# Optimization experiments

Measured on AMD Instinct MI355X. Metric: run time of the kernel, lower is better.

The kernel has to match this reference:

```python
import jax, jax.numpy as jnp
import numpy as np

B, N, C = 8, 4096, 256
HID = 256          # HGNN conv hidden width
MLP_HID = 64       # final_mlp_hidden_width


def setup_inputs() -> dict:
    key = jax.random.key(0)
    ks = jax.random.split(key, 10)
    s = lambda fan_in: 1.0 / np.sqrt(fan_in)
    states = jax.random.normal(ks[0], (B, N, C), dtype=jnp.float32)
    # symmetric-normalized hypergraph Laplacian-like propagation matrix [N, N]
    A = jax.random.uniform(ks[1], (N, N), dtype=jnp.float32)
    A = 0.5 * (A + A.T)
    d = jnp.sum(A, axis=1)
    G = A / jnp.sqrt(d[:, None] * d[None, :])
    W1 = jax.random.uniform(ks[2], (C, HID), jnp.float32, -s(C), s(C))
    b1 = jnp.zeros((HID,), jnp.float32)
    W2 = jax.random.uniform(ks[3], (HID, HID), jnp.float32, -s(HID), s(HID))
    b2 = jnp.zeros((HID,), jnp.float32)
    Wm1 = jax.random.uniform(ks[4], (HID, MLP_HID), jnp.float32, -s(HID), s(HID))
    bm1 = jnp.zeros((MLP_HID,), jnp.float32)
    Wm2 = jax.random.uniform(ks[5], (MLP_HID, 1), jnp.float32, -s(MLP_HID), s(MLP_HID))
    bm2 = jnp.zeros((1,), jnp.float32)
    return {"states": states, "G": G, "W1": W1, "b1": b1, "W2": W2,
            "b2": b2, "Wm1": Wm1, "bm1": bm1, "Wm2": Wm2, "bm2": bm2}


def reference(states, G, W1, b1, W2, b2, Wm1, bm1, Wm2, bm2):
    # HGNN conv 1: G @ (X W1 + b1), ReLU.  states: [B,N,C]
    h = jnp.einsum('nm,bmh->bnh', G, states @ W1 + b1)
    h = jax.nn.relu(h)
    # HGNN conv 2
    h = jnp.einsum('nm,bmh->bnh', G, h @ W2 + b2)
    h = jax.nn.relu(h)
    # final MLP: hidden -> 64 -> 1 (per-node scalar state value)
    h = jax.nn.relu(h @ Wm1 + bm1)
    return h @ Wm2 + bm2  # [B, N, 1]
```

## Files before the change

kernel.cpp:

```cpp
#include <hip/hip_runtime.h>

#define N_NODES 4096
#define C_IN    256
#define HID     256
#define BATCH   8
#define R_TOT   32768

typedef unsigned short u16;
typedef short s8v  __attribute__((ext_vector_type(8)));
typedef float f4v  __attribute__((ext_vector_type(4)));
typedef u16   u16x4 __attribute__((ext_vector_type(4)));

#define MFMA(a,b,c) __builtin_amdgcn_mfma_f32_16x16x32_bf16((a),(b),(c),0,0,0)

__device__ __forceinline__ u16 bf_rne(float x) {
    unsigned u = __float_as_uint(x);
    u += 0x7fffu + ((u >> 16) & 1u);
    return (u16)(u >> 16);
}
__device__ __forceinline__ float bf_f(u16 h) {
    return __uint_as_float(((unsigned)h) << 16);
}
__device__ __forceinline__ void split2f(float x, u16& h, u16& l) {
    h = bf_rne(x);
    l = bf_rne(x - bf_f(h));
}

__device__ __forceinline__ void glds16(const void* g, void* l) {
    __builtin_amdgcn_global_load_lds(
        (const __attribute__((address_space(1))) void*)g,
        (__attribute__((address_space(3))) void*)l, 16, 0, 0);
}


__global__ void splitGX_k(const float* __restrict__ G, u16* __restrict__ Gh,
                          const float* __restrict__ X, u16* __restrict__ Xh) {
    const int nG = 4194304;
    const int nTot = nG + 2097152;
    int i = blockIdx.x * blockDim.x + threadIdx.x;
    const int stride = gridDim.x * blockDim.x;
    for (; i < nTot; i += stride) {
        const float4* src; u16x4* dst; int j;
        if (i < nG) { src = (const float4*)G; dst = (u16x4*)Gh; j = i; }
        else        { src = (const float4*)X; dst = (u16x4*)Xh; j = i - nG; }
        float4 x = src[j];
        u16x4 hh;
        hh[0] = bf_rne(x.x); hh[1] = bf_rne(x.y);
        hh[2] = bf_rne(x.z); hh[3] = bf_rne(x.w);
        dst[j] = hh;
    }
}

__global__ void splitT2_k(const float* __restrict__ W1, u16* __restrict__ W1th,
                          u16* __restrict__ W1tl, const float* __restrict__ W2,
                          u16* __restrict__ W2th, u16* __restrict__ W2tl) {
    const float* in = blockIdx.y ? W2 : W1;
    u16* oh = blockIdx.y ? W2th : W1th;
    u16* ol = blockIdx.y ? W2tl : W1tl;
    const int c = blockIdx.x;
    const int h = threadIdx.x;
    float v = in[c * 256 + h];
    u16 hi, lo; split2f(v, hi, lo);
    oh[h * 256 + c] = hi;
    ol[h * 256 + c] = lo;
}

__global__ __launch_bounds__(256, 2) void gemm_small_k(
    const u16* __restrict__ Ah, const u16* __restrict__ Al,
    const u16* __restrict__ Bh,
    const float* __restrict__ bias, u16* __restrict__ Oh)
{
    __shared__ u16 sAh[4096], sAl[4096], sBh[4096];
    const int tid = threadIdx.x;
    const int w = tid >> 6, lane = tid & 63;
    const int i0 = blockIdx.x * 128;
    const int r0 = blockIdx.y * 128;
    const int lr = lane & 15, lk = lane >> 4;
    const int wr = (w >> 1) * 64, wc = (w & 1) * 64;
    const int kslot = (lk ^ ((lr >> 1) & 3)) * 8;
    const int cb = ((lane & 3) ^ ((lane >> 3) & 3)) * 8;

    const u16 *pAh[2], *pAl[2], *pBh[2];
#pragma unroll
    for (int j = 0; j < 2; ++j) {
        const int ra = i0 + (w * 2 + j) * 16 + (lane >> 2);
        pAh[j] = Ah + (size_t)ra * 256 + cb;
        pAl[j] = Al + (size_t)ra * 256 + cb;
        const int rb = r0 + (w * 2 + j) * 16 + (lane >> 2);
        pBh[j] = Bh + (size_t)rb * 256 + cb;
    }

    f4v acc[4][4] = {};

    for (int kt = 0; kt < 8; ++kt) {
#pragma unroll
        for (int j = 0; j < 2; ++j) {
            glds16(pAh[j] + kt * 32, sAh + (w * 2 + j) * 512);
            glds16(pAl[j] + kt * 32, sAl + (w * 2 + j) * 512);
            glds16(pBh[j] + kt * 32, sBh + (w * 2 + j) * 512);
        }
        __syncthreads();

        s8v fah[4], fal[4], fbh[4];
#pragma unroll
        for (int m = 0; m < 4; ++m) {
            fah[m] = *(const s8v*)(sAh + (wr + m * 16 + lr) * 32 + kslot);
            fal[m] = *(const s8v*)(sAl + (wr + m * 16 + lr) * 32 + kslot);
            fbh[m] = *(const s8v*)(sBh + (wc + m * 16 + lr) * 32 + kslot);
        }
#pragma unroll
        for (int m = 0; m < 4; ++m)
#pragma unroll
            for (int n = 0; n < 4; ++n)
                acc[m][n] = MFMA(fah[m], fbh[n], acc[m][n]);
#pragma unroll
        for (int m = 0; m < 4; ++m)
#pragma unroll
            for (int n = 0; n < 4; ++n)
                acc[m][n] = MFMA(fal[m], fbh[n], acc[m][n]);
        __syncthreads();
    }

#pragma unroll
    for (int m = 0; m < 4; ++m) {
#pragma unroll
        for (int q = 0; q < 4; ++q) {
            const int rowg = i0 + wr + m * 16 + lk * 4 + q;
            const float bv = bias[rowg];
#pragma unroll
            for (int n = 0; n < 4; ++n) {
                const int colg = r0 + wc + n * 16 + lr;
                float v = acc[m][n][q] + bv;
                Oh[(size_t)rowg * R_TOT + colg] = bf_rne(v);
            }
        }
    }
}

__global__ __launch_bounds__(512, 2) void gemm_big_k(
    const u16* __restrict__ Gh, const u16* __restrict__ Th,
    u16* __restrict__ Hh)
{
    extern __shared__ u16 lds[];
    const int tid = threadIdx.x;
    const int w = tid >> 6, l = tid & 63;
    const int n0 = blockIdx.x * 256;
    const int h0 = blockIdx.y * 128;
    const int b  = blockIdx.z;
    const int lr = l & 15, lk = l >> 4;
    const int wm = w >> 1, wn = w & 1;
    const int sl0 = ((lk)     ^ (lr & 7)) * 8;
    const int sl1 = ((4 + lk) ^ (lr & 7)) * 8;

    const int srow  = l >> 3;
    const int sslot = ((l & 7) ^ srow) * 8;

    const u16* pA0 = Gh + (size_t)(n0 + 8 * w        + srow) * 4096 + sslot;
    const u16* pA1 = Gh + (size_t)(n0 + 8 * (w + 8)  + srow) * 4096 + sslot;
    const u16* pA2 = Gh + (size_t)(n0 + 8 * (w + 16) + srow) * 4096 + sslot;
    const u16* pA3 = Gh + (size_t)(n0 + 8 * (w + 24) + srow) * 4096 + sslot;
    const u16* pB0 = Th + (size_t)(h0 + 8 * w       + srow) * R_TOT + (size_t)b * 4096 + sslot;
    const u16* pB1 = Th + (size_t)(h0 + 8 * (w + 8) + srow) * R_TOT + (size_t)b * 4096 + sslot;

    const int dA0 = w * 512, dA1 = (w + 8) * 512, dA2 = (w + 16) * 512, dA3 = (w + 24) * 512;
    const int dB0 = 16384 + w * 512, dB1 = 16384 + (w + 8) * 512;

    f4v acc[4][4] = {};

#define STAGE6(STG) do {                                                       \
    u16* Ls = lds + (STG) * 24576;                                             \
    glds16(pA0, Ls + dA0); glds16(pA1, Ls + dA1);                              \
    glds16(pA2, Ls + dA2); glds16(pA3, Ls + dA3);                              \
    glds16(pB0, Ls + dB0); glds16(pB1, Ls + dB1);                              \
    pA0 += 64; pA1 += 64; pA2 += 64; pA3 += 64; pB0 += 64; pB1 += 64;          \
} while (0)

#define KTILE(CUR, STG, DO_STAGE, VMODE) do {                                  \
    const u16* Lc = lds + (CUR) * 24576;                                       \
    u16* Ls = lds + (STG) * 24576;                                             \
                                  \
    { s8v fa[4], fb[4];                                                        \
      _Pragma("unroll") for (int m = 0; m < 4; ++m)                            \
          fa[m] = *(const s8v*)(Lc + (wm * 64 + m * 16 + lr) * 64 + sl0);      \
      _Pragma("unroll") for (int n = 0; n < 4; ++n)                            \
          fb[n] = *(const s8v*)(Lc + 16384 + (wn * 64 + n * 16 + lr) * 64 + sl0); \
      if (DO_STAGE) { glds16(pA0, Ls + dA0); glds16(pA1, Ls + dA1);            \
                      glds16(pB0, Ls + dB0); }                                 \
      __builtin_amdgcn_s_barrier();                                            \
      __builtin_amdgcn_s_setprio(1);                                           \
      _Pragma("unroll") for (int m = 0; m < 4; ++m)                            \
          _Pragma("unroll") for (int n = 0; n < 4; ++n)                        \
              acc[m][n] = MFMA(fa[m], fb[n], acc[m][n]);                       \
      __builtin_amdgcn_s_setprio(0);                                           \
      __builtin_amdgcn_s_barrier(); }                                          \
                     \
    { s8v fa[4], fb[4];                                                        \
      _Pragma("unroll") for (int m = 0; m < 4; ++m)                            \
          fa[m] = *(const s8v*)(Lc + (wm * 64 + m * 16 + lr) * 64 + sl1);      \
      _Pragma("unroll") for (int n = 0; n < 4; ++n)                            \
          fb[n] = *(const s8v*)(Lc + 16384 + (wn * 64 + n * 16 + lr) * 64 + sl1); \
      if (DO_STAGE) { glds16(pA2, Ls + dA2); glds16(pA3, Ls + dA3);            \
                      glds16(pB1, Ls + dB1);                                   \
                      pA0 += 64; pA1 += 64; pA2 += 64; pA3 += 64;              \
                      pB0 += 64; pB1 += 64; }                                  \
      __builtin_amdgcn_s_barrier();                                            \
      __builtin_amdgcn_s_setprio(1);                                           \
      _Pragma("unroll") for (int m = 0; m < 4; ++m)                            \
          _Pragma("unroll") for (int n = 0; n < 4; ++n)                        \
              acc[m][n] = MFMA(fa[m], fb[n], acc[m][n]);                       \
      __builtin_amdgcn_s_setprio(0); }                                         \
    if (VMODE == 0)      asm volatile("s_waitcnt vmcnt(6)" ::: "memory");      \
    else if (VMODE == 1) asm volatile("s_waitcnt vmcnt(0)" ::: "memory");      \
    if (VMODE != 2) __builtin_amdgcn_s_barrier();                              \
    __builtin_amdgcn_sched_barrier(0);                                         \
} while (0)

    STAGE6(0);
    STAGE6(1);
    asm volatile("s_waitcnt vmcnt(6)" ::: "memory");
    __builtin_amdgcn_s_barrier();
    __builtin_amdgcn_sched_barrier(0);

    for (int it = 0; it < 20; ++it) {
        KTILE(0, 2, 1, 0);
        KTILE(1, 0, 1, 0);
        KTILE(2, 1, 1, 0);
    }
    KTILE(0, 2, 1, 0);
    KTILE(1, 0, 1, 0);
    KTILE(2, 1, 0, 1);
    KTILE(0, 2, 0, 2);

#undef STAGE6
#undef KTILE

    const size_t obase = ((size_t)b * 4096 + n0 + wm * 64 + lk * 4) * 256
                       + h0 + wn * 64 + lr;
#pragma unroll
    for (int m = 0; m < 4; ++m)
#pragma unroll
        for (int n = 0; n < 4; ++n)
#pragma unroll
            for (int q = 0; q < 4; ++q) {
                float v = acc[m][n][q];
                v = v > 0.f ? v : 0.f;
                Hh[obase + (size_t)(m * 16 + q) * 256 + n * 16] = bf_rne(v);
            }
}

__global__ __launch_bounds__(256) void mlp_k(
    const u16* __restrict__ Hh, const float* __restrict__ Wm1,
    const float* __restrict__ bm1, const float* __restrict__ Wm2,
    const float* __restrict__ bm2, float* __restrict__ out)
{
    __shared__ u16 sB[16384];
    const int tid = threadIdx.x;
    const int w = tid >> 6, l = tid & 63;
    const int lr = l & 15, lk = l >> 4;

    for (int idx = tid; idx < 16384; idx += 256) {
        const int col = idx & 63, k = idx >> 6;
        const int slot = (k >> 3) ^ (col & 7);
        sB[col * 256 + slot * 8 + (k & 7)] = bf_rne(Wm1[k * 64 + col]);
    }
    __syncthreads();

    float bm1v[4], w2v[4];
#pragma unroll
    for (int n = 0; n < 4; ++n) {
        bm1v[n] = bm1[n * 16 + lr];
        w2v[n]  = Wm2[n * 16 + lr];
    }
    const float b2v = bm2[0];

    const int rowbase = blockIdx.x * 128 + w * 32;
    f4v acc[2][4] = {};
#pragma unroll
    for (int ks = 0; ks < 8; ++ks) {
        s8v fa[2], fb[4];
#pragma unroll
        for (int m = 0; m < 2; ++m)
            fa[m] = *(const s8v*)(Hh + (size_t)(rowbase + m * 16 + lr) * 256 + ks * 32 + lk * 8);
        const int slot = ((ks * 4 + lk) ^ (lr & 7)) * 8;
#pragma unroll
        for (int n = 0; n < 4; ++n)
            fb[n] = *(const s8v*)(sB + (n * 16 + lr) * 256 + slot);
#pragma unroll
        for (int m = 0; m < 2; ++m)
#pragma unroll
            for (int n = 0; n < 4; ++n)
                acc[m][n] = MFMA(fa[m], fb[n], acc[m][n]);
    }

#pragma unroll
    for (int m = 0; m < 2; ++m)
#pragma unroll
        for (int q = 0; q < 4; ++q) {
            float p = 0.f;
#pragma unroll
            for (int n = 0; n < 4; ++n) {
                float v = acc[m][n][q] + bm1v[n];
                v = v > 0.f ? v : 0.f;
                p += v * w2v[n];
            }
#pragma unroll
            for (int mask = 1; mask < 16; mask <<= 1)
                p += __shfl_xor(p, mask);
            if (lr == 0)
                out[rowbase + m * 16 + lk * 4 + q] = p + b2v;
        }
}

extern "C" void kernel_launch(void* const* d_in, const int* in_sizes, int n_in,
                              void* d_out, int out_size, void* d_ws, size_t ws_size,
                              hipStream_t stream) {
    (void)in_sizes; (void)n_in; (void)out_size; (void)ws_size;
    const float* X   = (const float*)d_in[0];
    const float* G   = (const float*)d_in[1];
    const float* W1  = (const float*)d_in[2];
    const float* b1  = (const float*)d_in[3];
    const float* W2  = (const float*)d_in[4];
    const float* b2  = (const float*)d_in[5];
    const float* Wm1 = (const float*)d_in[6];
    const float* bm1 = (const float*)d_in[7];
    const float* Wm2 = (const float*)d_in[8];
    const float* bm2 = (const float*)d_in[9];
    float* out = (float*)d_out;

    char* ws = (char*)d_ws;
    u16* Gh   = (u16*)(ws);
    u16* W1th = (u16*)(ws + 67108864u);
    u16* W1tl = (u16*)(ws + 67239936u);
    u16* W2th = (u16*)(ws + 67371008u);
    u16* W2tl = (u16*)(ws + 67502080u);
    u16* Tth  = (u16*)(ws + 67633152u);
    u16* XHh  = (u16*)(ws + 101187584u);

    splitGX_k<<<3072, 256, 0, stream>>>(G, Gh, X, XHh);
    splitT2_k<<<dim3(256, 2), 256, 0, stream>>>(W1, W1th, W1tl, W2, W2th, W2tl);

    gemm_small_k<<<dim3(2, 256), 256, 0, stream>>>(W1th, W1tl, XHh, b1, Tth);
    gemm_big_k<<<dim3(16, 2, 8), 512, 147456, stream>>>(Gh, Tth, XHh);
    gemm_small_k<<<dim3(2, 256), 256, 0, stream>>>(W2th, W2tl, XHh, b2, Tth);
    gemm_big_k<<<dim3(16, 2, 8), 512, 147456, stream>>>(Gh, Tth, XHh);
    mlp_k<<<256, 256, 0, stream>>>(XHh, Wm1, bm1, Wm2, bm2, out);
}
```

Before: 191.1 us.

## Load B operand directly from global into registers, keep only A in LDS

New measurement: 367.4 us. +92.2%, slower.

```diff
diff --git a/kernel.cpp b/kernel.cpp
--- a/kernel.cpp
+++ b/kernel.cpp
@@ -155,83 +155,92 @@
     const int srow  = l >> 3;
     const int sslot = ((l & 7) ^ srow) * 8;
 
-    const u16* pA0 = Gh + (size_t)(n0 + 8 * w        + srow) * 4096 + sslot;
-    const u16* pA1 = Gh + (size_t)(n0 + 8 * (w + 8)  + srow) * 4096 + sslot;
-    const u16* pA2 = Gh + (size_t)(n0 + 8 * (w + 16) + srow) * 4096 + sslot;
-    const u16* pA3 = Gh + (size_t)(n0 + 8 * (w + 24) + srow) * 4096 + sslot;
-    const u16* pB0 = Th + (size_t)(h0 + 8 * w       + srow) * R_TOT + (size_t)b * 4096 + sslot;
-    const u16* pB1 = Th + (size_t)(h0 + 8 * (w + 8) + srow) * R_TOT + (size_t)b * 4096 + sslot;
-
+    const u16* pA0 = Gh + (size_t)(n0 + 8 * w + srow) * 4096 + sslot;
+    const u16* pA1 = pA0 + (size_t)64  * 4096;
+    const u16* pA2 = pA0 + (size_t)128 * 4096;
+    const u16* pA3 = pA0 + (size_t)192 * 4096;
     const int dA0 = w * 512, dA1 = (w + 8) * 512, dA2 = (w + 16) * 512, dA3 = (w + 24) * 512;
-    const int dB0 = 16384 + w * 512, dB1 = 16384 + (w + 8) * 512;
+
+    const u16* pB[4];
+#pragma unroll
+    for (int n = 0; n < 4; ++n)
+        pB[n] = Th + (size_t)(h0 + wn * 64 + n * 16 + lr) * R_TOT
+                   + (size_t)b * 4096 + lk * 8;
 
     f4v acc[4][4] = {};
-
-#define STAGE6(STG) do {                                                       \
-    u16* Ls = lds + (STG) * 24576;                                             \
+    s8v bbA[8], bbB[8];
+
+#define STAGEA(STG) do {                                                       \
+    u16* Ls = lds + (STG) * 16384;                                             \
     glds16(pA0, Ls + dA0); glds16(pA1, Ls + dA1);                              \
     glds16(pA2, Ls + dA2); glds16(pA3, Ls + dA3);                              \
-    glds16(pB0, Ls + dB0); glds16(pB1, Ls + dB1);                              \
-    pA0 += 64; pA1 += 64; pA2 += 64; pA3 += 64; pB0 += 64; pB1 += 64;          \
+    pA0 += 64; pA1 += 64; pA2 += 64; pA3 += 64;                                \
 } while (0)
 
-#define KTILE(CUR, STG, DO_STAGE, VMODE) do {                                  \
-    const u16* Lc = lds + (CUR) * 24576;                                       \
-    u16* Ls = lds + (STG) * 24576;                                             \
-                                  \
-    { s8v fa[4], fb[4];                                                        \
+#define KTILE(CUR, STG, BBC, BBN, DO_STAGE, DO_B, VMODE) do {                  \
+    const u16* Lc = lds + (CUR) * 16384;                                       \
+                           \
+    { s8v fa[4];                                                               \
       _Pragma("unroll") for (int m = 0; m < 4; ++m)                            \
           fa[m] = *(const s8v*)(Lc + (wm * 64 + m * 16 + lr) * 64 + sl0);      \
-      _Pragma("unroll") for (int n = 0; n < 4; ++n)                            \
-          fb[n] = *(const s8v*)(Lc + 16384 + (wn * 64 + n * 16 + lr) * 64 + sl0); \
-      if (DO_STAGE) { glds16(pA0, Ls + dA0); glds16(pA1, Ls + dA1);            \
-                      glds16(pB0, Ls + dB0); }                                 \
+      if (DO_B) {                                                              \
+          _Pragma("unroll") for (int n = 0; n < 4; ++n)                        \
+              BBN[n] = *(const s8v*)(pB[n] + 64);                              \
+      }                                                                        \
       __builtin_amdgcn_s_barrier();                                            \
       __builtin_amdgcn_s_setprio(1);                                           \
       _Pragma("unroll") for (int m = 0; m < 4; ++m)                            \
           _Pragma("unroll") for (int n = 0; n < 4; ++n)                        \
-              acc[m][n] = MFMA(fa[m], fb[n], acc[m][n]);                       \
+              acc[m][n] = MFMA(fa[m], BBC[n], acc[m][n]);                      \
       __builtin_amdgcn_s_setprio(0);                                           \
       __builtin_amdgcn_s_barrier(); }                                          \
-                     \
-    { s8v fa[4], fb[4];                                                        \
+             \
+    { s8v fa[4];                                                               \
       _Pragma("unroll") for (int m = 0; m < 4; ++m)                            \
           fa[m] = *(const s8v*)(Lc + (wm * 64 + m * 16 + lr) * 64 + sl1);      \
-      _Pragma("unroll") for (int n = 0; n < 4; ++n)                            \
-          fb[n] = *(const s8v*)(Lc + 16384 + (wn * 64 + n * 16 + lr) * 64 + sl1); \
-      if (DO_STAGE) { glds16(pA2, Ls + dA2); glds16(pA3, Ls + dA3);            \
-                      glds16(pB1, Ls + dB1);                                   \
-                      pA0 += 64; pA1 += 64; pA2 += 64; pA3 += 64;              \
-                      pB0 += 64; pB1 += 64; }                                  \
+      if (DO_STAGE) STAGEA(STG);                                               \
+      if (DO_B) {                                                              \
+          _Pragma("unroll") for (int n = 0; n < 4; ++n)                        \
+              BBN[4 + n] = *(const s8v*)(pB[n] + 96);                          \
+      }                                                                        \
       __builtin_amdgcn_s_barrier();                                            \
       __builtin_amdgcn_s_setprio(1);                                           \
       _Pragma("unroll") for (int m = 0; m < 4; ++m)                            \
           _Pragma("unroll") for (int n = 0; n < 4; ++n)                        \
-              acc[m][n] = MFMA(fa[m], fb[n], acc[m][n]);                       \
+              acc[m][n] = MFMA(fa[m], BBC[4 + n], acc[m][n]);                  \
       __builtin_amdgcn_s_setprio(0); }                                         \
-    if (VMODE == 0)      asm volatile("s_waitcnt vmcnt(6)" ::: "memory");      \
-    else if (VMODE == 1) asm volatile("s_waitcnt vmcnt(0)" ::: "memory");      \
+    if (DO_B) { _Pragma("unroll") for (int n = 0; n < 4; ++n) pB[n] += 64; }   \
+    __builtin_amdgcn_sched_barrier(0);                                         \
+    if (VMODE == 0)      asm volatile("s_waitcnt vmcnt(16)" ::: "memory");     \
+    else if (VMODE == 1) asm volatile("s_waitcnt vmcnt(12)" ::: "memory");     \
     if (VMODE != 2) __builtin_amdgcn_s_barrier();                              \
     __builtin_amdgcn_sched_barrier(0);                                         \
 } while (0)
 
-    STAGE6(0);
-    STAGE6(1);
-    asm volatile("s_waitcnt vmcnt(6)" ::: "memory");
+    STAGEA(0);
+    STAGEA(1);
+#pragma unroll
+    for (int n = 0; n < 4; ++n) bbA[n]     = *(const s8v*)(pB[n]);
+#pragma unroll
+    for (int n = 0; n < 4; ++n) bbA[4 + n] = *(const s8v*)(pB[n] + 32);
+    asm volatile("s_waitcnt vmcnt(12)" ::: "memory");
     __builtin_amdgcn_s_barrier();
     __builtin_amdgcn_sched_barrier(0);
 
-    for (int it = 0; it < 20; ++it) {
-        KTILE(0, 2, 1, 0);
-        KTILE(1, 0, 1, 0);
-        KTILE(2, 1, 1, 0);
-    }
-    KTILE(0, 2, 1, 0);
-    KTILE(1, 0, 1, 0);
-    KTILE(2, 1, 0, 1);
-    KTILE(0, 2, 0, 2);
-
-#undef STAGE6
+    for (int it = 0; it < 10; ++it) {
+        KTILE(0, 2, bbA, bbB, 1, 1, 0);
+        KTILE(1, 0, bbB, bbA, 1, 1, 0);
+        KTILE(2, 1, bbA, bbB, 1, 1, 0);
+        KTILE(0, 2, bbB, bbA, 1, 1, 0);
+        KTILE(1, 0, bbA, bbB, 1, 1, 0);
+        KTILE(2, 1, bbB, bbA, 1, 1, 0);
+    }
+    KTILE(0, 2, bbA, bbB, 1, 1, 0);
+    KTILE(1, 0, bbB, bbA, 1, 1, 0);
+    KTILE(2, 1, bbA, bbB, 0, 1, 1);
+    KTILE(0, 2, bbB, bbA, 0, 0, 2);
+
+#undef STAGEA
 #undef KTILE
 
     const size_t obase = ((size_t)b * 4096 + n0 + wm * 64 + lk * 4) * 256
@@ -340,8 +349,8 @@
     splitT2_k<<<dim3(256, 2), 256, 0, stream>>>(W1, W1th, W1tl, W2, W2th, W2tl);
 
     gemm_small_k<<<dim3(2, 256), 256, 0, stream>>>(W1th, W1tl, XHh, b1, Tth);
-    gemm_big_k<<<dim3(16, 2, 8), 512, 147456, stream>>>(Gh, Tth, XHh);
+    gemm_big_k<<<dim3(16, 2, 8), 512, 98304, stream>>>(Gh, Tth, XHh);
     gemm_small_k<<<dim3(2, 256), 256, 0, stream>>>(W2th, W2tl, XHh, b2, Tth);
-    gemm_big_k<<<dim3(16, 2, 8), 512, 147456, stream>>>(Gh, Tth, XHh);
+    gemm_big_k<<<dim3(16, 2, 8), 512, 98304, stream>>>(Gh, Tth, XHh);
     mlp_k<<<256, 256, 0, stream>>>(XHh, Wm1, bm1, Wm2, bm2, out);
 }
```
